# Kernel optimization log

Hardware: AMD Instinct MI355X
Metric: run time of the kernel (lower is better)

The kernel has to match this reference:

```python
import jax, jax.numpy as jnp
import numpy as np

ALPHA = 0.5  # leakage
T, B, I, H = 512, 64, 128, 1024
SCALE = 0.9  # input_scaling
RHO = 0.99   # target spectral radius (approximated by 1/sqrt(H) normal scaling)


def setup_inputs() -> dict:
    key = jax.random.key(0)
    k1, k2, k3, k4, k5 = jax.random.split(key, 5)
    x = jax.random.normal(k1, (T, B, I), dtype=jnp.float32)
    # uniform(-scale, scale) kernel init
    W_in0 = jax.random.uniform(k2, (H, I), jnp.float32, -SCALE, SCALE)
    # normal recurrent init scaled so spectral radius ~= rho (circular law: radius ~ sigma*sqrt(H))
    W_hat0 = jax.random.normal(k3, (H, H), jnp.float32) * (RHO / np.sqrt(H))
    W_in1 = jax.random.uniform(k4, (H, H), jnp.float32, -SCALE, SCALE)
    W_hat1 = jax.random.normal(k5, (H, H), jnp.float32) * (RHO / np.sqrt(H))
    return {"x": x, "W_in0": W_in0, "W_hat0": W_hat0, "W_in1": W_in1, "W_hat1": W_hat1}


def _run_layer(inp, W_in, W_hat):
    # inp: [T, B, F_in]; returns full state trajectory [T, B, H]
    def step(h, x_t):
        pre = x_t @ W_in.T + h @ W_hat.T          # [B, H]
        h_new = (1.0 - ALPHA) * h + ALPHA * jnp.tanh(pre)
        return h_new, h_new

    h0 = jnp.zeros((inp.shape[1], W_hat.shape[0]), dtype=inp.dtype)
    _, ys = jax.lax.scan(step, h0, inp)
    return ys


def reference(x, W_in0, W_hat0, W_in1, W_hat1):
    e0 = _run_layer(x, W_in0, W_hat0)   # layer 0 states [T, B, H]
    e1 = _run_layer(e0, W_in1, W_hat1)  # layer 1 states [T, B, H]
    return jnp.stack([e0, e1], axis=-2)  # [T, B, num_layers, H]
```

## Files before the change

### kernel.cpp

```cpp
#include <hip/hip_runtime.h>
#include <math.h>

#define TSTEPS 512
#define BATCH  64
#define HDIM   1024
#define IDIM   128
#define NBLOCKS 256
#define NTHR   512

typedef __attribute__((ext_vector_type(8))) short bf16x8;
typedef __attribute__((ext_vector_type(4))) float f32x4;
typedef __attribute__((ext_vector_type(4))) unsigned u32x4;

#define WI0HI 0
#define WI0LO (WI0HI + 1024*128)
#define WH0HI (WI0LO + 1024*128)
#define WH0LO (WH0HI + 1024*1024)
#define WI1HI (WH0LO + 1024*1024)
#define WI1LO (WI1HI + 1024*1024)
#define WH1HI (WI1LO + 1024*1024)
#define WH1LO (WH1HI + 1024*1024)
#define WS_USHORTS (WH1LO + 1024*1024)
#define CNT_OFF_BYTES ((size_t)WS_USHORTS * 2)
#define FLG_DW (256 * 16)
#define BAR_BYTES (3 * 256 * 64)

__device__ __forceinline__ unsigned short bf_hi(float f) {
    unsigned u = __builtin_bit_cast(unsigned, f);
    unsigned r = u + 0x7fffu + ((u >> 16) & 1u);
    return (unsigned short)(r >> 16);
}
__device__ __forceinline__ float bf_tof(unsigned short h) {
    unsigned u = ((unsigned)h) << 16;
    return __builtin_bit_cast(float, u);
}

__device__ __forceinline__ void split8v(f32x4 a, f32x4 b,
                                        bf16x8& ah, bf16x8& al) {
    float fv[8] = {a[0], a[1], a[2], a[3], b[0], b[1], b[2], b[3]};
    u32x4 H, L;
    #pragma unroll
    for (int q = 0; q < 4; ++q) {
        const float f0 = fv[2 * q], f1 = fv[2 * q + 1];
        unsigned h;
        asm("v_cvt_pk_bf16_f32 %0, %1, %2" : "=v"(h) : "v"(f0), "v"(f1));
        const float h0 = __builtin_bit_cast(float, h << 16);
        const float h1 = __builtin_bit_cast(float, h & 0xffff0000u);
        unsigned lo;
        asm("v_cvt_pk_bf16_f32 %0, %1, %2" : "=v"(lo) : "v"(f0 - h0), "v"(f1 - h1));
        H[q] = h; L[q] = lo;
    }
    ah = __builtin_bit_cast(bf16x8, H);
    al = __builtin_bit_cast(bf16x8, L);
}

__device__ __forceinline__ void ks_r2(f32x4 a, f32x4 b,
                                      bf16x8 bh, bf16x8 bl, f32x4& acc) {
    bf16x8 ah, al;
    split8v(a, b, ah, al);
    acc = __builtin_amdgcn_mfma_f32_16x16x32_bf16(ah, bh, acc, 0, 0, 0);
    acc = __builtin_amdgcn_mfma_f32_16x16x32_bf16(al, bh, acc, 0, 0, 0);
    acc = __builtin_amdgcn_mfma_f32_16x16x32_bf16(ah, bl, acc, 0, 0, 0);
}

#define LDG4(B, base, g) _Pragma("unroll") for (int c = 0; c < 4; ++c) { \
    (B)[2*c]   = *(const f32x4*)((base) + ((g)*4 + c) * 32); \
    (B)[2*c+1] = *(const f32x4*)((base) + ((g)*4 + c) * 32 + 4); }
#define PROC4(B, wOff, g) _Pragma("unroll") for (int c = 0; c < 4; ++c) { \
    ks_r2((B)[2*c], (B)[2*c+1], wfh[(wOff)+(g)*4+c], wfl[(wOff)+(g)*4+c], \
          ((((g)*4+c) & 1) ? accA : accB)); }

__global__ void prep_kernel(const float* __restrict__ Wi0, const float* __restrict__ Wh0,
                            const float* __restrict__ Wi1, const float* __restrict__ Wh1,
                            unsigned short* __restrict__ wsU)
{
    const int n = 1024*128 + 3*1024*1024;
    for (int e = blockIdx.x * blockDim.x + threadIdx.x; e < n;
         e += gridDim.x * blockDim.x) {
        const float* src; int idx, hiOff, loOff;
        if (e < 1024*128)            { src = Wi0; idx = e;              hiOff = WI0HI; loOff = WI0LO; }
        else if (e < 1024*128 + 1024*1024)   { src = Wh0; idx = e - 1024*128;   hiOff = WH0HI; loOff = WH0LO; }
        else if (e < 1024*128 + 2*1024*1024) { src = Wi1; idx = e - 1024*128 - 1024*1024; hiOff = WI1HI; loOff = WI1LO; }
        else                         { src = Wh1; idx = e - 1024*128 - 2*1024*1024; hiOff = WH1HI; loOff = WH1LO; }
        float f = src[idx];
        unsigned short h = bf_hi(f);
        wsU[hiOff + idx] = h;
        wsU[loOff + idx] = bf_hi(f - bf_tof(h));
    }
}

__device__ __forceinline__ void barrier_arrive(unsigned* cnt, unsigned epoch) {
    __syncthreads();
    if (threadIdx.x == 0)
        __hip_atomic_store(cnt + (unsigned)blockIdx.x * 16, epoch,
                           __ATOMIC_RELAXED, __HIP_MEMORY_SCOPE_AGENT);
}
__device__ __forceinline__ void barrier_wait(unsigned* cnt, unsigned epoch, int layer) {
    const int tid = (int)threadIdx.x;
    const int bid = (int)blockIdx.x;
    if ((bid & 127) == 0) {
        if (tid < 64) {
            unsigned* arr = cnt + layer * (128 * 16);
            for (;;) {
                unsigned v0 = __hip_atomic_load(arr + (tid     ) * 16, __ATOMIC_RELAXED, __HIP_MEMORY_SCOPE_AGENT);
                unsigned v1 = __hip_atomic_load(arr + (tid + 64) * 16, __ATOMIC_RELAXED, __HIP_MEMORY_SCOPE_AGENT);
                bool ok = (v0 >= epoch) & (v1 >= epoch);
                if (__ballot(ok) == ~0ull) break;
                __builtin_amdgcn_s_sleep(1);
            }
            unsigned* flg = cnt + FLG_DW + layer * 4096;
            #pragma unroll
            for (int q = 0; q < 4; ++q)
                __hip_atomic_store(flg + (q * 64 + tid) * 16, epoch,
                                   __ATOMIC_RELAXED, __HIP_MEMORY_SCOPE_AGENT);
        }
        if (layer == 1 && tid == 0) {
            unsigned* f0 = cnt + FLG_DW + (unsigned)bid * 16;
            while (__hip_atomic_load(f0, __ATOMIC_RELAXED,
                                     __HIP_MEMORY_SCOPE_AGENT) < epoch)
                __builtin_amdgcn_s_sleep(1);
        }
    } else if (tid == 0) {
        unsigned* f0 = cnt + FLG_DW + (unsigned)bid * 16;
        if (layer == 0) {
            while (__hip_atomic_load(f0, __ATOMIC_RELAXED,
                                     __HIP_MEMORY_SCOPE_AGENT) < epoch)
                __builtin_amdgcn_s_sleep(1);
        } else {
            unsigned* f1 = cnt + FLG_DW + 4096 + (unsigned)bid * 16;
            for (;;) {
                unsigned a = __hip_atomic_load(f1, __ATOMIC_RELAXED, __HIP_MEMORY_SCOPE_AGENT);
                unsigned b = __hip_atomic_load(f0, __ATOMIC_RELAXED, __HIP_MEMORY_SCOPE_AGENT);
                if (a >= epoch && b >= epoch) break;
                __builtin_amdgcn_s_sleep(1);
            }
        }
    }
    __syncthreads();
}

__global__ __launch_bounds__(NTHR, 2) void reservoir_kernel(
    const float* __restrict__ x, float* __restrict__ out,
    const unsigned short* __restrict__ wsU, unsigned* __restrict__ cnt)
{
    __shared__ f32x4 red[8 * 64];

    const int bid = blockIdx.x;
    const int layer = bid >> 7;
    const int rr  = bid & 127;
    const int jt  = rr >> 1, mh = rr & 1;
    const int tid = (int)threadIdx.x;
    const int w   = __builtin_amdgcn_readfirstlane(tid >> 6);
    const int m2  = w & 1, kh = w >> 1;
    const int l   = tid & 63, lr = l & 15, tq = l >> 4;
    const int jbase = jt * 16;
    const int arow  = mh * 32 + m2 * 16 + lr;

    bf16x8 wfh[16], wfl[16];
    if (layer == 0) {
        const size_t rx = (size_t)(jbase + lr) * IDIM + kh * 32 + tq * 8;
        wfh[0] = *(const bf16x8*)(wsU + WI0HI + rx);
        wfl[0] = *(const bf16x8*)(wsU + WI0LO + rx);
        const size_t rh = (size_t)(jbase + lr) * HDIM + kh * 256 + tq * 8;
        #pragma unroll
        for (int ks = 0; ks < 8; ++ks) {
            wfh[1 + ks] = *(const bf16x8*)(wsU + WH0HI + rh + ks * 32);
            wfl[1 + ks] = *(const bf16x8*)(wsU + WH0LO + rh + ks * 32);
        }
    } else {
        const int hiOff = (kh < 2) ? WI1HI : WH1HI;
        const int loOff = (kh < 2) ? WI1LO : WH1LO;
        const size_t ro = (size_t)(jbase + lr) * HDIM + (kh & 1) * 512 + tq * 8;
        #pragma unroll
        for (int ks = 0; ks < 16; ++ks) {
            wfh[ks] = *(const bf16x8*)(wsU + hiOff + ro + ks * 32);
            wfl[ks] = *(const bf16x8*)(wsU + loOff + ro + ks * 32);
        }
    }

    const int rowLocal = tid >> 4;
    const int colF = tid & 15;
    const int m2f = rowLocal >> 4, tqf = (rowLocal >> 2) & 3, rf = rowLocal & 3;
    const int lf  = tqf * 16 + colF;
    float hold = 0.f;
    f32x4 accX = {0.f, 0.f, 0.f, 0.f};

    for (int i = 0; i <= TSTEPS; ++i) {
        const int t = layer ? (i - 1) : i;
        const bool valid = layer ? (t >= 0) : (t < TSTEPS);
        if (valid) {
            f32x4 accA = {0.f, 0.f, 0.f, 0.f};
            f32x4 accB = {0.f, 0.f, 0.f, 0.f};
            if (layer == 0) {
                if (i == 0) {
                    f32x4 xa = *(const f32x4*)(x + (size_t)t * (BATCH * IDIM) + arow * IDIM + kh * 32 + tq * 8);
                    f32x4 xb = *(const f32x4*)(x + (size_t)t * (BATCH * IDIM) + arow * IDIM + kh * 32 + tq * 8 + 4);
                    ks_r2(xa, xb, wfh[0], wfl[0], accA);
                } else {
                    accA = accX;
                }
                if (t >= 1) {
                    const float* h0 = out + (size_t)(t - 1) * 131072 + arow * 2048
                                      + kh * 256 + tq * 8;
                    f32x4 bA[8], bB[8];
                    LDG4(bA, h0, 0);
                    LDG4(bB, h0, 1);
                    PROC4(bA, 1, 0);
                    PROC4(bB, 1, 1);
                }
            } else {
                const bool doit = (kh < 2) || (t >= 1);
                if (doit) {
                    const int ts  = (kh < 2) ? t : (t - 1);
                    const float* src = out + (size_t)ts * 131072 + arow * 2048
                                       + ((kh < 2) ? 0 : 1024) + (kh & 1) * 512 + tq * 8;
                    f32x4 bA[8], bB[8];
                    LDG4(bA, src, 0);
                    LDG4(bB, src, 1);
                    PROC4(bA, 0, 0);
                    LDG4(bA, src, 2);
                    PROC4(bB, 0, 1);
                    LDG4(bB, src, 3);
                    PROC4(bA, 0, 2);
                    PROC4(bB, 0, 3);
                }
            }

            red[w * 64 + l] = accA + accB;
            __syncthreads();
            {
                float s = 0.f;
                #pragma unroll
                for (int k4 = 0; k4 < 4; ++k4)
                    s += red[(k4 * 2 + m2f) * 64 + lf][rf];
                const float hnew = 0.5f * hold + 0.5f * tanhf(s);
                hold = hnew;
                const int row = mh * 32 + rowLocal;
                float* dst = out + (size_t)t * 131072 + row * 2048 + layer * 1024 + jbase + colF;
                __hip_atomic_store(dst, hnew, __ATOMIC_RELAXED, __HIP_MEMORY_SCOPE_AGENT);
            }
            __syncthreads();
        }
        if (i < TSTEPS) {
            barrier_arrive(cnt, (unsigned)(i + 1));
            if (layer == 0 && (i + 1) < TSTEPS) {
                const float* xs = x + (size_t)(i + 1) * (BATCH * IDIM) + arow * IDIM + kh * 32 + tq * 8;
                f32x4 xa = *(const f32x4*)(xs);
                f32x4 xb = *(const f32x4*)(xs + 4);
                f32x4 z = {0.f, 0.f, 0.f, 0.f};
                ks_r2(xa, xb, wfh[0], wfl[0], z);
                accX = z;
            }
            barrier_wait(cnt, (unsigned)(i + 1), layer);
        }
    }
}

extern "C" void kernel_launch(void* const* d_in, const int* in_sizes, int n_in,
                              void* d_out, int out_size, void* d_ws, size_t ws_size,
                              hipStream_t stream) {
    const float* x   = (const float*)d_in[0];
    const float* Wi0 = (const float*)d_in[1];
    const float* Wh0 = (const float*)d_in[2];
    const float* Wi1 = (const float*)d_in[3];
    const float* Wh1 = (const float*)d_in[4];
    float* out = (float*)d_out;
    unsigned short* wsU = (unsigned short*)d_ws;
    unsigned* cnt = (unsigned*)((char*)d_ws + CNT_OFF_BYTES);

    hipMemsetAsync((char*)d_ws + CNT_OFF_BYTES, 0, BAR_BYTES, stream);
    prep_kernel<<<256, 256, 0, stream>>>(Wi0, Wh0, Wi1, Wh1, wsU);

    void* args[] = {(void*)&x, (void*)&out, (void*)&wsU, (void*)&cnt};
    hipLaunchCooperativeKernel((const void*)reservoir_kernel,
                               dim3(NBLOCKS), dim3(NTHR), args, 0, stream);
}
```

Before: 4.620 ms.

## Double threads per block and split the K reduction across 16 waves

Each block now runs 1024 threads (16 waves) in place of 512, so every wave handles half the K range. Per-wave weight registers and per-step MFMA work are halved, and the LDS cross-wave reduction grows from 4 to 8 partials per output. The aim is to shorten the per-timestep critical path in this latency-bound recurrent scan by spreading the matvec over more waves. In exchange the block-level syncs cost more, the reduction is longer, and half the threads sit idle during the tanh/store phase.

```diff
diff --git a/kernel.cpp b/kernel.cpp
--- a/kernel.cpp
+++ b/kernel.cpp
@@ -6,7 +6,7 @@
 #define HDIM   1024
 #define IDIM   128
 #define NBLOCKS 256
-#define NTHR   512
+#define NTHR   1024
 
 typedef __attribute__((ext_vector_type(8))) short bf16x8;
 typedef __attribute__((ext_vector_type(4))) float f32x4;
@@ -63,12 +63,12 @@
     acc = __builtin_amdgcn_mfma_f32_16x16x32_bf16(ah, bl, acc, 0, 0, 0);
 }
 
-#define LDG4(B, base, g) _Pragma("unroll") for (int c = 0; c < 4; ++c) { \
-    (B)[2*c]   = *(const f32x4*)((base) + ((g)*4 + c) * 32); \
-    (B)[2*c+1] = *(const f32x4*)((base) + ((g)*4 + c) * 32 + 4); }
-#define PROC4(B, wOff, g) _Pragma("unroll") for (int c = 0; c < 4; ++c) { \
-    ks_r2((B)[2*c], (B)[2*c+1], wfh[(wOff)+(g)*4+c], wfl[(wOff)+(g)*4+c], \
-          ((((g)*4+c) & 1) ? accA : accB)); }
+#define LD2(B, base, g) _Pragma("unroll") for (int c = 0; c < 2; ++c) { \
+    (B)[2*c]   = *(const f32x4*)((base) + ((g)*2 + c) * 32); \
+    (B)[2*c+1] = *(const f32x4*)((base) + ((g)*2 + c) * 32 + 4); }
+#define PR2(B, g) _Pragma("unroll") for (int c = 0; c < 2; ++c) { \
+    ks_r2((B)[2*c], (B)[2*c+1], wfh[(g)*2+c], wfl[(g)*2+c], \
+          ((((g)*2+c) & 1) ? accA : accB)); }
 
 __global__ void prep_kernel(const float* __restrict__ Wi0, const float* __restrict__ Wh0,
                             const float* __restrict__ Wi1, const float* __restrict__ Wh1,
@@ -139,11 +139,11 @@
     __syncthreads();
 }
 
-__global__ __launch_bounds__(NTHR, 2) void reservoir_kernel(
+__global__ __launch_bounds__(NTHR, 4) void reservoir_kernel(
     const float* __restrict__ x, float* __restrict__ out,
     const unsigned short* __restrict__ wsU, unsigned* __restrict__ cnt)
 {
-    __shared__ f32x4 red[8 * 64];
+    __shared__ f32x4 red[16 * 64];
 
     const int bid = blockIdx.x;
     const int layer = bid >> 7;
@@ -156,25 +156,28 @@
     const int jbase = jt * 16;
     const int arow  = mh * 32 + m2 * 16 + lr;
 
-    bf16x8 wfh[16], wfl[16];
+    bf16x8 wfh[8], wfl[8];
+    bf16x8 wxh = {}, wxl = {};
     if (layer == 0) {
-        const size_t rx = (size_t)(jbase + lr) * IDIM + kh * 32 + tq * 8;
-        wfh[0] = *(const bf16x8*)(wsU + WI0HI + rx);
-        wfl[0] = *(const bf16x8*)(wsU + WI0LO + rx);
-        const size_t rh = (size_t)(jbase + lr) * HDIM + kh * 256 + tq * 8;
+        const size_t rh = (size_t)(jbase + lr) * HDIM + kh * 128 + tq * 8;
         #pragma unroll
-        for (int ks = 0; ks < 8; ++ks) {
-            wfh[1 + ks] = *(const bf16x8*)(wsU + WH0HI + rh + ks * 32);
-            wfl[1 + ks] = *(const bf16x8*)(wsU + WH0LO + rh + ks * 32);
+        for (int c = 0; c < 4; ++c) {
+            wfh[c] = *(const bf16x8*)(wsU + WH0HI + rh + c * 32);
+            wfl[c] = *(const bf16x8*)(wsU + WH0LO + rh + c * 32);
+        }
+        if (kh < 4) {
+            const size_t rx = (size_t)(jbase + lr) * IDIM + kh * 32 + tq * 8;
+            wxh = *(const bf16x8*)(wsU + WI0HI + rx);
+            wxl = *(const bf16x8*)(wsU + WI0LO + rx);
         }
     } else {
-        const int hiOff = (kh < 2) ? WI1HI : WH1HI;
-        const int loOff = (kh < 2) ? WI1LO : WH1LO;
-        const size_t ro = (size_t)(jbase + lr) * HDIM + (kh & 1) * 512 + tq * 8;
+        const int hiOff = (kh < 4) ? WI1HI : WH1HI;
+        const int loOff = (kh < 4) ? WI1LO : WH1LO;
+        const size_t ro = (size_t)(jbase + lr) * HDIM + (kh & 3) * 256 + tq * 8;
         #pragma unroll
-        for (int ks = 0; ks < 16; ++ks) {
-            wfh[ks] = *(const bf16x8*)(wsU + hiOff + ro + ks * 32);
-            wfl[ks] = *(const bf16x8*)(wsU + loOff + ro + ks * 32);
+        for (int c = 0; c < 8; ++c) {
+            wfh[c] = *(const bf16x8*)(wsU + hiOff + ro + c * 32);
+            wfl[c] = *(const bf16x8*)(wsU + loOff + ro + c * 32);
         }
     }
 
@@ -192,47 +195,41 @@
             f32x4 accA = {0.f, 0.f, 0.f, 0.f};
             f32x4 accB = {0.f, 0.f, 0.f, 0.f};
             if (layer == 0) {
-                if (i == 0) {
-                    f32x4 xa = *(const f32x4*)(x + (size_t)t * (BATCH * IDIM) + arow * IDIM + kh * 32 + tq * 8);
-                    f32x4 xb = *(const f32x4*)(x + (size_t)t * (BATCH * IDIM) + arow * IDIM + kh * 32 + tq * 8 + 4);
-                    ks_r2(xa, xb, wfh[0], wfl[0], accA);
-                } else {
-                    accA = accX;
+                if (kh < 4) {
+                    if (i == 0) {
+                        const float* xs = x + (size_t)t * (BATCH * IDIM) + arow * IDIM + kh * 32 + tq * 8;
+                        ks_r2(*(const f32x4*)xs, *(const f32x4*)(xs + 4), wxh, wxl, accA);
+                    } else {
+                        accA = accX;
+                    }
                 }
                 if (t >= 1) {
                     const float* h0 = out + (size_t)(t - 1) * 131072 + arow * 2048
-                                      + kh * 256 + tq * 8;
-                    f32x4 bA[8], bB[8];
-                    LDG4(bA, h0, 0);
-                    LDG4(bB, h0, 1);
-                    PROC4(bA, 1, 0);
-                    PROC4(bB, 1, 1);
+                                      + kh * 128 + tq * 8;
+                    f32x4 bA[4], bB[4];
+                    LD2(bA, h0, 0); LD2(bB, h0, 1);
+                    PR2(bA, 0); PR2(bB, 1);
                 }
             } else {
-                const bool doit = (kh < 2) || (t >= 1);
-                if (doit) {
-                    const int ts  = (kh < 2) ? t : (t - 1);
+                if ((kh < 4) || (t >= 1)) {
+                    const int ts  = (kh < 4) ? t : (t - 1);
                     const float* src = out + (size_t)ts * 131072 + arow * 2048
-                                       + ((kh < 2) ? 0 : 1024) + (kh & 1) * 512 + tq * 8;
-                    f32x4 bA[8], bB[8];
-                    LDG4(bA, src, 0);
-                    LDG4(bB, src, 1);
-                    PROC4(bA, 0, 0);
-                    LDG4(bA, src, 2);
-                    PROC4(bB, 0, 1);
-                    LDG4(bB, src, 3);
-                    PROC4(bA, 0, 2);
-                    PROC4(bB, 0, 3);
+                                       + ((kh < 4) ? 0 : 1024) + (kh & 3) * 256 + tq * 8;
+                    f32x4 bA[4], bB[4];
+                    LD2(bA, src, 0); LD2(bB, src, 1);
+                    PR2(bA, 0); LD2(bA, src, 2);
+                    PR2(bB, 1); LD2(bB, src, 3);
+                    PR2(bA, 2); PR2(bB, 3);
                 }
             }
 
             red[w * 64 + l] = accA + accB;
             __syncthreads();
-            {
+            if (tid < 512) {
                 float s = 0.f;
                 #pragma unroll
-                for (int k4 = 0; k4 < 4; ++k4)
-                    s += red[(k4 * 2 + m2f) * 64 + lf][rf];
+                for (int k8 = 0; k8 < 8; ++k8)
+                    s += red[(k8 * 2 + m2f) * 64 + lf][rf];
                 const float hnew = 0.5f * hold + 0.5f * tanhf(s);
                 hold = hnew;
                 const int row = mh * 32 + rowLocal;
@@ -243,12 +240,10 @@
         }
         if (i < TSTEPS) {
             barrier_arrive(cnt, (unsigned)(i + 1));
-            if (layer == 0 && (i + 1) < TSTEPS) {
+            if (layer == 0 && kh < 4 && (i + 1) < TSTEPS) {
                 const float* xs = x + (size_t)(i + 1) * (BATCH * IDIM) + arow * IDIM + kh * 32 + tq * 8;
-                f32x4 xa = *(const f32x4*)(xs);
-                f32x4 xb = *(const f32x4*)(xs + 4);
                 f32x4 z = {0.f, 0.f, 0.f, 0.f};
-                ks_r2(xa, xb, wfh[0], wfl[0], z);
+                ks_r2(*(const f32x4*)xs, *(const f32x4*)(xs + 4), wxh, wxl, z);
                 accX = z;
             }
             barrier_wait(cnt, (unsigned)(i + 1), layer);
```

Result: slower. 6.142 ms (+33.0%).

## Replace centralized grid barrier with per-batch-half domain barriers and finer load pipelining

Applied to the files above, without the earlier changes.

Removes the master-block barrier that gathered all 128 per-layer arrival flags and rebroadcast them. Blocks now sync only within their batch-half domain (layer, mh), since rows of one mh depend only on the same rows of the previous step. Every block polls the 64 domain flags directly, and layer 1 also polls layer 0's matching domain. The global loads of h are split into smaller double-buffered chunks of 2 k-steps interleaved with MFMA, which cuts register use and overlaps loads with compute. The cost is more polling traffic from every block.

```diff
diff --git a/kernel.cpp b/kernel.cpp
--- a/kernel.cpp
+++ b/kernel.cpp
@@ -22,8 +22,7 @@
 #define WH1LO (WH1HI + 1024*1024)
 #define WS_USHORTS (WH1LO + 1024*1024)
 #define CNT_OFF_BYTES ((size_t)WS_USHORTS * 2)
-#define FLG_DW (256 * 16)
-#define BAR_BYTES (3 * 256 * 64)
+#define BAR_BYTES (256 * 64)
 
 __device__ __forceinline__ unsigned short bf_hi(float f) {
     unsigned u = __builtin_bit_cast(unsigned, f);
@@ -63,12 +62,12 @@
     acc = __builtin_amdgcn_mfma_f32_16x16x32_bf16(ah, bl, acc, 0, 0, 0);
 }
 
-#define LDG4(B, base, g) _Pragma("unroll") for (int c = 0; c < 4; ++c) { \
-    (B)[2*c]   = *(const f32x4*)((base) + ((g)*4 + c) * 32); \
-    (B)[2*c+1] = *(const f32x4*)((base) + ((g)*4 + c) * 32 + 4); }
-#define PROC4(B, wOff, g) _Pragma("unroll") for (int c = 0; c < 4; ++c) { \
-    ks_r2((B)[2*c], (B)[2*c+1], wfh[(wOff)+(g)*4+c], wfl[(wOff)+(g)*4+c], \
-          ((((g)*4+c) & 1) ? accA : accB)); }
+#define LD2(B, base, g) _Pragma("unroll") for (int c = 0; c < 2; ++c) { \
+    (B)[2*c]   = *(const f32x4*)((base) + ((g)*2 + c) * 32); \
+    (B)[2*c+1] = *(const f32x4*)((base) + ((g)*2 + c) * 32 + 4); }
+#define PR2(B, wOff, g) _Pragma("unroll") for (int c = 0; c < 2; ++c) { \
+    ks_r2((B)[2*c], (B)[2*c+1], wfh[(wOff)+(g)*2+c], wfl[(wOff)+(g)*2+c], \
+          ((((g)*2+c) & 1) ? accA : accB)); }
 
 __global__ void prep_kernel(const float* __restrict__ Wi0, const float* __restrict__ Wh0,
                             const float* __restrict__ Wi1, const float* __restrict__ Wh1,
@@ -89,49 +88,34 @@
     }
 }
 
-__device__ __forceinline__ void barrier_arrive(unsigned* cnt, unsigned epoch) {
+__device__ __forceinline__ void barrier_arrive(unsigned* cnt, unsigned epoch,
+                                               int dom, int jt) {
     __syncthreads();
     if (threadIdx.x == 0)
-        __hip_atomic_store(cnt + (unsigned)blockIdx.x * 16, epoch,
+        __hip_atomic_store(cnt + (unsigned)(dom * 64 + jt) * 16, epoch,
                            __ATOMIC_RELAXED, __HIP_MEMORY_SCOPE_AGENT);
 }
-__device__ __forceinline__ void barrier_wait(unsigned* cnt, unsigned epoch, int layer) {
+__device__ __forceinline__ void barrier_wait(unsigned* cnt, unsigned epoch,
+                                             int layer, int mh) {
     const int tid = (int)threadIdx.x;
-    const int bid = (int)blockIdx.x;
-    if ((bid & 127) == 0) {
-        if (tid < 64) {
-            unsigned* arr = cnt + layer * (128 * 16);
+    if (tid < 64) {
+        const int dom = layer * 2 + mh;
+        unsigned* own = cnt + (unsigned)(dom * 64 + tid) * 16;
+        if (layer == 0) {
             for (;;) {
-                unsigned v0 = __hip_atomic_load(arr + (tid     ) * 16, __ATOMIC_RELAXED, __HIP_MEMORY_SCOPE_AGENT);
-                unsigned v1 = __hip_atomic_load(arr + (tid + 64) * 16, __ATOMIC_RELAXED, __HIP_MEMORY_SCOPE_AGENT);
-                bool ok = (v0 >= epoch) & (v1 >= epoch);
-                if (__ballot(ok) == ~0ull) break;
+                unsigned v = __hip_atomic_load(own, __ATOMIC_RELAXED,
+                                               __HIP_MEMORY_SCOPE_AGENT);
+                if (__ballot(v >= epoch) == ~0ull) break;
                 __builtin_amdgcn_s_sleep(1);
             }
-            unsigned* flg = cnt + FLG_DW + layer * 4096;
-            #pragma unroll
-            for (int q = 0; q < 4; ++q)
-                __hip_atomic_store(flg + (q * 64 + tid) * 16, epoch,
-                                   __ATOMIC_RELAXED, __HIP_MEMORY_SCOPE_AGENT);
-        }
-        if (layer == 1 && tid == 0) {
-            unsigned* f0 = cnt + FLG_DW + (unsigned)bid * 16;
-            while (__hip_atomic_load(f0, __ATOMIC_RELAXED,
-                                     __HIP_MEMORY_SCOPE_AGENT) < epoch)
-                __builtin_amdgcn_s_sleep(1);
-        }
-    } else if (tid == 0) {
-        unsigned* f0 = cnt + FLG_DW + (unsigned)bid * 16;
-        if (layer == 0) {
-            while (__hip_atomic_load(f0, __ATOMIC_RELAXED,
-                                     __HIP_MEMORY_SCOPE_AGENT) < epoch)
-                __builtin_amdgcn_s_sleep(1);
         } else {
-            unsigned* f1 = cnt + FLG_DW + 4096 + (unsigned)bid * 16;
+            unsigned* up = cnt + (unsigned)(mh * 64 + tid) * 16;
             for (;;) {
-                unsigned a = __hip_atomic_load(f1, __ATOMIC_RELAXED, __HIP_MEMORY_SCOPE_AGENT);
-                unsigned b = __hip_atomic_load(f0, __ATOMIC_RELAXED, __HIP_MEMORY_SCOPE_AGENT);
-                if (a >= epoch && b >= epoch) break;
+                unsigned a = __hip_atomic_load(own, __ATOMIC_RELAXED,
+                                               __HIP_MEMORY_SCOPE_AGENT);
+                unsigned b = __hip_atomic_load(up, __ATOMIC_RELAXED,
+                                               __HIP_MEMORY_SCOPE_AGENT);
+                if (__ballot((a >= epoch) & (b >= epoch)) == ~0ull) break;
                 __builtin_amdgcn_s_sleep(1);
             }
         }
@@ -149,6 +133,7 @@
     const int layer = bid >> 7;
     const int rr  = bid & 127;
     const int jt  = rr >> 1, mh = rr & 1;
+    const int dom = layer * 2 + mh;
     const int tid = (int)threadIdx.x;
     const int w   = __builtin_amdgcn_readfirstlane(tid >> 6);
     const int m2  = w & 1, kh = w >> 1;
@@ -202,27 +187,26 @@
                 if (t >= 1) {
                     const float* h0 = out + (size_t)(t - 1) * 131072 + arow * 2048
                                       + kh * 256 + tq * 8;
-                    f32x4 bA[8], bB[8];
-                    LDG4(bA, h0, 0);
-                    LDG4(bB, h0, 1);
-                    PROC4(bA, 1, 0);
-                    PROC4(bB, 1, 1);
+                    f32x4 bA[4], bB[4];
+                    LD2(bA, h0, 0); LD2(bB, h0, 1);
+                    PR2(bA, 1, 0); LD2(bA, h0, 2);
+                    PR2(bB, 1, 1); LD2(bB, h0, 3);
+                    PR2(bA, 1, 2); PR2(bB, 1, 3);
                 }
             } else {
-                const bool doit = (kh < 2) || (t >= 1);
-                if (doit) {
+                if ((kh < 2) || (t >= 1)) {
                     const int ts  = (kh < 2) ? t : (t - 1);
                     const float* src = out + (size_t)ts * 131072 + arow * 2048
                                        + ((kh < 2) ? 0 : 1024) + (kh & 1) * 512 + tq * 8;
-                    f32x4 bA[8], bB[8];
-                    LDG4(bA, src, 0);
-                    LDG4(bB, src, 1);
-                    PROC4(bA, 0, 0);
-                    LDG4(bA, src, 2);
-                    PROC4(bB, 0, 1);
-                    LDG4(bB, src, 3);
-                    PROC4(bA, 0, 2);
-                    PROC4(bB, 0, 3);
+                    f32x4 bA[4], bB[4];
+                    LD2(bA, src, 0); LD2(bB, src, 1);
+                    PR2(bA, 0, 0); LD2(bA, src, 2);
+                    PR2(bB, 0, 1); LD2(bB, src, 3);
+                    PR2(bA, 0, 2); LD2(bA, src, 4);
+                    PR2(bB, 0, 3); LD2(bB, src, 5);
+                    PR2(bA, 0, 4); LD2(bA, src, 6);
+                    PR2(bB, 0, 5); LD2(bB, src, 7);
+                    PR2(bA, 0, 6); PR2(bB, 0, 7);
                 }
             }
 
@@ -242,7 +226,7 @@
             __syncthreads();
         }
         if (i < TSTEPS) {
-            barrier_arrive(cnt, (unsigned)(i + 1));
+            barrier_arrive(cnt, (unsigned)(i + 1), dom, jt);
             if (layer == 0 && (i + 1) < TSTEPS) {
                 const float* xs = x + (size_t)(i + 1) * (BATCH * IDIM) + arow * IDIM + kh * 32 + tq * 8;
                 f32x4 xa = *(const f32x4*)(xs);
@@ -251,7 +235,7 @@
                 ks_r2(xa, xb, wfh[0], wfl[0], z);
                 accX = z;
             }
-            barrier_wait(cnt, (unsigned)(i + 1), layer);
+            barrier_wait(cnt, (unsigned)(i + 1), layer, mh);
         }
     }
 }
```

Measured after the change: 4.408 ms, median of 2. 4.6% less time.
